# Optimization experiments

Measured on AMD Instinct MI355X. Metric: run time of the kernel, lower is better.

The kernel has to match this reference:

```python
import jax, jax.numpy as jnp
import numpy as np

TOP_K = 2  # num_experts_per_token


def setup_inputs() -> dict:
    key = jax.random.key(0)
    ks = jax.random.split(key, 6)
    B, S, H, F, E = 4, 2048, 1024, 4096, 8  # F = 2 * intermediate_size
    scale = 0.02
    x = jax.random.normal(ks[0], (B, S, H), dtype=jnp.float32)
    gate_w = jax.random.normal(ks[1], (E, H), dtype=jnp.float32) * scale
    w1 = jax.random.normal(ks[2], (E, H, F), dtype=jnp.float32) * scale
    b1 = jnp.zeros((E, F), dtype=jnp.float32)
    w2 = jax.random.normal(ks[3], (E, F, H), dtype=jnp.float32) * scale
    b2 = jnp.zeros((E, H), dtype=jnp.float32)
    return {"x": x, "gate_w": gate_w, "w1": w1, "b1": b1, "w2": w2, "b2": b2}


def reference(x, gate_w, w1, b1, w2, b2):
    # x: [B, S, H]; gate_w: [E, H]; w1: [E, H, F]; b1: [E, F]; w2: [E, F, H]; b2: [E, H]
    E = gate_w.shape[0]
    gate_logits = jnp.einsum('bsh,eh->bse', x, gate_w)
    gate_probs = jax.nn.softmax(gate_logits, axis=-1)
    top_v, top_i = jax.lax.top_k(gate_probs, TOP_K)  # [B, S, K]
    # Combine weight per expert: w[b,s,e] = sum_k top_v[b,s,k] * (top_i[b,s,k] == e)
    onehot = jax.nn.one_hot(top_i, E, dtype=x.dtype)          # [B, S, K, E]
    comb_w = jnp.einsum('bsk,bske->bse', top_v, onehot)       # [B, S, E]
    out = jnp.zeros_like(x)
    for e in range(E):  # small fixed expert loop
        h = jax.nn.silu(jnp.einsum('bsh,hf->bsf', x, w1[e]) + b1[e])
        y = jnp.einsum('bsf,fh->bsh', h, w2[e]) + b2[e]
        out = out + y * comb_w[..., e:e + 1]
    return out
```

## Files before the change

### kernel.cpp

```cpp
#include <hip/hip_runtime.h>
#include <stdint.h>

#define T_TOK 8192
#define HDIM  1024
#define FDIM  4096
#define NEXP  8
#define BT    256
#define RCAP  (2*T_TOK + NEXP*256)
#define LDSB  65536

typedef short  short8  __attribute__((ext_vector_type(8)));
typedef unsigned short ushort8 __attribute__((ext_vector_type(8)));
typedef float  f32x4   __attribute__((ext_vector_type(4)));

#define MFMA __builtin_amdgcn_mfma_f32_16x16x32_bf16

__device__ __forceinline__ unsigned short f2bf(float f) {
  unsigned u = __float_as_uint(f);
  u += 0x7fffu + ((u >> 16) & 1u);
  return (unsigned short)(u >> 16);
}
__device__ __forceinline__ float bf2f(unsigned short u) {
  return __uint_as_float((unsigned)u << 16);
}

__device__ __forceinline__ void gload16(const void* g, void* l) {
  __builtin_amdgcn_global_load_lds(
      (const __attribute__((address_space(1))) void*)g,
      (__attribute__((address_space(3))) void*)l, 16, 0, 0);
}

__global__ __launch_bounds__(256) void k_transp_cvt(const float* __restrict__ in,
                                                    unsigned short* __restrict__ out,
                                                    int K, int N) {
  __shared__ unsigned short s[64][72];
  const float* ine = in + (size_t)blockIdx.z * K * N;
  unsigned short* oute = out + (size_t)blockIdx.z * K * N;
  int k0 = blockIdx.y * 64, n0 = blockIdx.x * 64;
  int t = threadIdx.x;
  int kr = t >> 4, nc = (t & 15) * 4;
#pragma unroll
  for (int it = 0; it < 4; ++it) {
    int k = it * 16 + kr;
    float4 v = *(const float4*)(ine + (size_t)(k0 + k) * N + n0 + nc);
    ushort4 u = make_ushort4(f2bf(v.x), f2bf(v.y), f2bf(v.z), f2bf(v.w));
    *(ushort4*)(&s[k][nc]) = u;
  }
  __syncthreads();
  int nr = t >> 3, kc = (t & 7) * 8;
#pragma unroll
  for (int v = 0; v < 2; ++v) {
    int n = v * 32 + nr;
    ushort8 o;
#pragma unroll
    for (int j = 0; j < 8; ++j) o[j] = s[kc + j][n];
    *(ushort8*)(oute + (size_t)(n0 + n) * K + k0 + kc) = o;
  }
}

__global__ void k_gate(const float* __restrict__ x, const float* __restrict__ gw,
                       unsigned short* __restrict__ xb,
                       int2* __restrict__ eidx, float2* __restrict__ ewt) {
  int tid = threadIdx.x;
  int lane = tid & 63;
  int t = blockIdx.x * 4 + (tid >> 6);
  const float* xr = x + (size_t)t * HDIM;
  unsigned short* xbr = xb + (size_t)t * HDIM;
  float acc[NEXP];
#pragma unroll
  for (int e = 0; e < NEXP; e++) acc[e] = 0.f;
#pragma unroll
  for (int i = 0; i < HDIM / 64; i++) {
    float xv = xr[i * 64 + lane];
    xbr[i * 64 + lane] = f2bf(xv);
#pragma unroll
    for (int e = 0; e < NEXP; e++) acc[e] += xv * gw[e * HDIM + i * 64 + lane];
  }
#pragma unroll
  for (int e = 0; e < NEXP; e++) {
    acc[e] += __shfl_xor(acc[e], 32);
    acc[e] += __shfl_xor(acc[e], 16);
    acc[e] += __shfl_xor(acc[e], 8);
    acc[e] += __shfl_xor(acc[e], 4);
    acc[e] += __shfl_xor(acc[e], 2);
    acc[e] += __shfl_xor(acc[e], 1);
  }
  float m = acc[0];
#pragma unroll
  for (int e = 1; e < NEXP; e++) m = fmaxf(m, acc[e]);
  float p[NEXP]; float s = 0.f;
#pragma unroll
  for (int e = 0; e < NEXP; e++) { p[e] = expf(acc[e] - m); s += p[e]; }
  float inv = 1.f / s;
#pragma unroll
  for (int e = 0; e < NEXP; e++) p[e] *= inv;
  int b0 = 0; float v0 = p[0];
#pragma unroll
  for (int e = 1; e < NEXP; e++) if (p[e] > v0) { v0 = p[e]; b0 = e; }
  int b1i = (b0 == 0) ? 1 : 0; float v1 = p[b1i];
#pragma unroll
  for (int e = 0; e < NEXP; e++) if (e != b0 && p[e] > v1) { v1 = p[e]; b1i = e; }
  if (lane == 0) { eidx[t] = make_int2(b0, b1i); ewt[t] = make_float2(v0, v1); }
}

__global__ void k_compact(const int2* __restrict__ eidx,
                          int* __restrict__ list_tok, int* __restrict__ counts) {
  int e = blockIdx.x;
  int tid = threadIdx.x, lane = tid & 63, wid = tid >> 6;
  __shared__ int sbase;
  __shared__ int wcnt[4];
  if (tid == 0) sbase = 0;
  __syncthreads();
  for (int c = 0; c < T_TOK; c += 256) {
    int t = c + tid;
    int2 ei = eidx[t];
    bool sel = (ei.x == e) || (ei.y == e);
    unsigned long long b = __ballot(sel);
    if (lane == 0) wcnt[wid] = __popcll(b);
    __syncthreads();
    int pre = sbase;
    for (int w = 0; w < wid; w++) pre += wcnt[w];
    int pos = pre + __popcll(b & ((1ull << lane) - 1ull));
    if (sel) list_tok[e * T_TOK + pos] = t;
    __syncthreads();
    if (tid == 0) sbase += wcnt[0] + wcnt[1] + wcnt[2] + wcnt[3];
    __syncthreads();
  }
  if (tid == 0) counts[e] = sbase;
}

__global__ void k_offsets(const int* __restrict__ counts, int* __restrict__ off_pad) {
  if (threadIdx.x == 0) {
    int o = 0;
    off_pad[0] = 0;
    for (int e = 0; e < NEXP; e++) {
      o += ((counts[e] + BT - 1) / BT) * BT;
      off_pad[e + 1] = o;
    }
  }
}

__global__ void k_invert(const int* __restrict__ list_tok, const int* __restrict__ counts,
                         const int* __restrict__ off_pad, const int2* __restrict__ eidx,
                         int2* __restrict__ tok2slot) {
  int e = blockIdx.y;
  int p = blockIdx.x * 256 + threadIdx.x;
  if (p < counts[e]) {
    int t = list_tok[e * T_TOK + p];
    int slot = off_pad[e] + p;
    if (eidx[t].x == e) tok2slot[t].x = slot;
    else                tok2slot[t].y = slot;
  }
}

#define STAGE_A(u_, v_) { \
    char* lb_ = smem + (((v_)&1) ? LDSB : 0) + (u_)*16384; \
    gload16(gA[u_][0] + (size_t)(v_)*128, lb_ + dst0); \
    gload16(gA[u_][1] + (size_t)(v_)*128, lb_ + dst1); }
#define STAGE_B(u_, v_) { \
    char* lb_ = smem + (((v_)&1) ? LDSB : 0) + 32768 + (u_)*16384; \
    gload16(gB[u_][0] + (size_t)(v_)*128, lb_ + dst0); \
    gload16(gB[u_][1] + (size_t)(v_)*128, lb_ + dst1); }

#define PHASE2(M0_, M1_, M2_, M3_, STAGE_STMT, TAIL_STMT) { \
    short8 a0l = *(const short8*)(pA0 + (M0_)*2048), a0h = *(const short8*)(pA1 + (M0_)*2048); \
    short8 a1l = *(const short8*)(pA0 + (M1_)*2048), a1h = *(const short8*)(pA1 + (M1_)*2048); \
    short8 a2l = *(const short8*)(pA0 + (M2_)*2048), a2h = *(const short8*)(pA1 + (M2_)*2048); \
    short8 a3l = *(const short8*)(pA0 + (M3_)*2048), a3h = *(const short8*)(pA1 + (M3_)*2048); \
    STAGE_STMT; \
    __builtin_amdgcn_s_barrier(); \
    asm volatile("s_waitcnt lgkmcnt(0)" ::: "memory"); \
    __builtin_amdgcn_sched_barrier(0); \
    __builtin_amdgcn_s_setprio(1); \
    acc[M0_][0] = MFMA(a0l, b00, acc[M0_][0], 0,0,0); \
    acc[M0_][1] = MFMA(a0l, b10, acc[M0_][1], 0,0,0); \
    acc[M0_][2] = MFMA(a0l, b20, acc[M0_][2], 0,0,0); \
    acc[M0_][3] = MFMA(a0l, b30, acc[M0_][3], 0,0,0); \
    acc[M1_][0] = MFMA(a1l, b00, acc[M1_][0], 0,0,0); \
    acc[M1_][1] = MFMA(a1l, b10, acc[M1_][1], 0,0,0); \
    acc[M1_][2] = MFMA(a1l, b20, acc[M1_][2], 0,0,0); \
    acc[M1_][3] = MFMA(a1l, b30, acc[M1_][3], 0,0,0); \
    acc[M2_][0] = MFMA(a2l, b00, acc[M2_][0], 0,0,0); \
    acc[M2_][1] = MFMA(a2l, b10, acc[M2_][1], 0,0,0); \
    acc[M2_][2] = MFMA(a2l, b20, acc[M2_][2], 0,0,0); \
    acc[M2_][3] = MFMA(a2l, b30, acc[M2_][3], 0,0,0); \
    acc[M3_][0] = MFMA(a3l, b00, acc[M3_][0], 0,0,0); \
    acc[M3_][1] = MFMA(a3l, b10, acc[M3_][1], 0,0,0); \
    acc[M3_][2] = MFMA(a3l, b20, acc[M3_][2], 0,0,0); \
    acc[M3_][3] = MFMA(a3l, b30, acc[M3_][3], 0,0,0); \
    acc[M0_][0] = MFMA(a0h, b01, acc[M0_][0], 0,0,0); \
    acc[M0_][1] = MFMA(a0h, b11, acc[M0_][1], 0,0,0); \
    acc[M0_][2] = MFMA(a0h, b21, acc[M0_][2], 0,0,0); \
    acc[M0_][3] = MFMA(a0h, b31, acc[M0_][3], 0,0,0); \
    acc[M1_][0] = MFMA(a1h, b01, acc[M1_][0], 0,0,0); \
    acc[M1_][1] = MFMA(a1h, b11, acc[M1_][1], 0,0,0); \
    acc[M1_][2] = MFMA(a1h, b21, acc[M1_][2], 0,0,0); \
    acc[M1_][3] = MFMA(a1h, b31, acc[M1_][3], 0,0,0); \
    acc[M2_][0] = MFMA(a2h, b01, acc[M2_][0], 0,0,0); \
    acc[M2_][1] = MFMA(a2h, b11, acc[M2_][1], 0,0,0); \
    acc[M2_][2] = MFMA(a2h, b21, acc[M2_][2], 0,0,0); \
    acc[M2_][3] = MFMA(a2h, b31, acc[M2_][3], 0,0,0); \
    acc[M3_][0] = MFMA(a3h, b01, acc[M3_][0], 0,0,0); \
    acc[M3_][1] = MFMA(a3h, b11, acc[M3_][1], 0,0,0); \
    acc[M3_][2] = MFMA(a3h, b21, acc[M3_][2], 0,0,0); \
    acc[M3_][3] = MFMA(a3h, b31, acc[M3_][3], 0,0,0); \
    __builtin_amdgcn_s_setprio(0); \
    TAIL_STMT; \
    __builtin_amdgcn_s_barrier(); }

#define READ_B4 \
    short8 b00 = *(const short8*)(pB0),        b01 = *(const short8*)(pB1); \
    short8 b10 = *(const short8*)(pB0 + 2048), b11 = *(const short8*)(pB1 + 2048); \
    short8 b20 = *(const short8*)(pB0 + 4096), b21 = *(const short8*)(pB1 + 4096); \
    short8 b30 = *(const short8*)(pB0 + 6144), b31 = *(const short8*)(pB1 + 6144);

#define GEMM_TILE_LOOP(NT) \
  STAGE_A(0,0); STAGE_A(1,0); STAGE_B(0,0); STAGE_B(1,0); STAGE_B(0,1); STAGE_B(1,1); \
  asm volatile("s_waitcnt vmcnt(4)" ::: "memory"); \
  __builtin_amdgcn_s_barrier(); \
  for (int v = 0; v < (NT); ++v) { \
    const char* bufb = smem + ((v&1) ? LDSB : 0); \
    const char* pA0 = bufb + wm * 16384 + aoff0; \
    const char* pA1 = bufb + wm * 16384 + aoff1; \
    const char* pB0 = bufb + 32768 + (wn >> 1) * 16384 + boff0; \
    const char* pB1 = bufb + 32768 + (wn >> 1) * 16384 + boff1; \
    READ_B4; \
    PHASE2(0, 1, 2, 3, { if (v+1 < (NT)) { STAGE_A(0, v+1); STAGE_A(1, v+1); } }, {}); \
    PHASE2(4, 5, 6, 7, { if (v+2 < (NT)) { STAGE_B(0, v+2); STAGE_B(1, v+2); } }, { \
      if (v+2 < (NT))      { asm volatile("s_waitcnt vmcnt(4)" ::: "memory"); } \
      else if (v+1 < (NT)) { asm volatile("s_waitcnt vmcnt(0)" ::: "memory"); } }); \
  }

__global__ __launch_bounds__(512, 2) void k_gemm1(
    const unsigned short* __restrict__ xb, const unsigned short* __restrict__ w1t,
    const float* __restrict__ b1, const int* __restrict__ list_tok,
    const int* __restrict__ counts, const int* __restrict__ off_pad,
    unsigned short* __restrict__ h) {
  extern __shared__ char smem[];
  int wl = (blockIdx.x & 7) * 144 + (blockIdx.x >> 3);
  int r0 = (wl >> 4) * BT;
  int n0 = (wl & 15) * BT;
  if (r0 >= off_pad[NEXP]) return;
  int e = 0;
#pragma unroll
  for (int i = 0; i < NEXP; ++i) if (r0 >= off_pad[i + 1]) e = i + 1;
  int base = off_pad[e], cnt = counts[e];

  int t = threadIdx.x, l = t & 63, w = t >> 6;
  int wm = w >> 2, wn = w & 3;
  int lr = l & 15, g16 = (l >> 4) * 16;
  int swz = (lr & 7) << 4;
  int aoff0 = lr * 128 + (g16 ^ swz);
  int aoff1 = lr * 128 + ((64 + g16) ^ swz);
  int boff0 = (wn & 1) * 8192 + aoff0;
  int boff1 = (wn & 1) * 8192 + aoff1;

  int dst0 = t * 16, dst1 = t * 16 + 8192;
  int srow = t >> 3;
  int skb = (((t & 7) ^ ((t >> 3) & 7)) << 4);
  const char* gA[2][2];
  const char* gB[2][2];
#pragma unroll
  for (int u = 0; u < 2; ++u)
#pragma unroll
    for (int j = 0; j < 2; ++j) {
      int row = u * 128 + srow + 64 * j;
      int se = r0 - base + row;
      int tok = (se < cnt) ? list_tok[e * T_TOK + se] : 0;
      gA[u][j] = (const char*)(xb + (size_t)tok * HDIM) + skb;
      gB[u][j] = (const char*)(w1t + (size_t)e * FDIM * HDIM + (size_t)(n0 + row) * HDIM) + skb;
    }

  f32x4 acc[8][4];
#pragma unroll
  for (int m = 0; m < 8; ++m)
#pragma unroll
    for (int n = 0; n < 4; ++n) acc[m][n] = (f32x4){0.f, 0.f, 0.f, 0.f};

  GEMM_TILE_LOOP(HDIM / 64);

  const float* b1e = b1 + (size_t)e * FDIM + n0;
  unsigned short* Cs = (unsigned short*)smem;
  int lh = l >> 4, lh4 = lh * 4;
  int cswz = lh << 4;
#pragma unroll
  for (int n = 0; n < 4; ++n) {
    int col = wn * 64 + n * 16 + lr;
    int colX = col ^ cswz;
    float bv = b1e[col];
#pragma unroll
    for (int m = 0; m < 8; ++m) {
      int row = wm * 128 + m * 16 + lh4;
#pragma unroll
      for (int i = 0; i < 4; ++i) {
        float vv = acc[m][n][i] + bv;
        float sg = __builtin_amdgcn_rcpf(1.f + __expf(-vv));
        Cs[(size_t)(row + i) * BT + colX] = f2bf(vv * sg);
      }
    }
  }
  __syncthreads();
#pragma unroll
  for (int s = 0; s < 16; ++s) {
    int lin = s * 512 + t;
    int row = lin >> 5, c8 = (lin & 31) * 8;
    int c8X = c8 ^ (((row >> 2) & 3) << 4);
    *(ushort8*)(h + (size_t)(r0 + row) * FDIM + n0 + c8) = *(const ushort8*)(Cs + (size_t)row * BT + c8X);
  }
}

__global__ __launch_bounds__(512, 2) void k_gemm2(
    const unsigned short* __restrict__ h, const unsigned short* __restrict__ w2t,
    const float* __restrict__ b2, const int* __restrict__ off_pad,
    unsigned short* __restrict__ ypartA, unsigned short* __restrict__ ypartB) {
  extern __shared__ char smem[];
  int wl = (blockIdx.x & 7) * 72 + (blockIdx.x >> 3);
  int mB = wl >> 3, rem = wl & 7;
  int r0 = mB * BT;
  int n0 = (rem >> 1) * BT;
  int z  = rem & 1;
  if (r0 >= off_pad[NEXP]) return;
  int e = 0;
#pragma unroll
  for (int i = 0; i < NEXP; ++i) if (r0 >= off_pad[i + 1]) e = i + 1;

  int t = threadIdx.x, l = t & 63, w = t >> 6;
  int wm = w >> 2, wn = w & 3;
  int lr = l & 15, g16 = (l >> 4) * 16;
  int swz = (lr & 7) << 4;
  int aoff0 = lr * 128 + (g16 ^ swz);
  int aoff1 = lr * 128 + ((64 + g16) ^ swz);
  int boff0 = (wn & 1) * 8192 + aoff0;
  int boff1 = (wn & 1) * 8192 + aoff1;

  int dst0 = t * 16, dst1 = t * 16 + 8192;
  int srow = t >> 3;
  int skb = (((t & 7) ^ ((t >> 3) & 7)) << 4);
  const char* gA[2][2];
  const char* gB[2][2];
#pragma unroll
  for (int u = 0; u < 2; ++u)
#pragma unroll
    for (int j = 0; j < 2; ++j) {
      int row = u * 128 + srow + 64 * j;
      gA[u][j] = (const char*)(h + (size_t)(r0 + row) * FDIM + (size_t)z * 2048) + skb;
      gB[u][j] = (const char*)(w2t + (size_t)e * HDIM * FDIM + (size_t)(n0 + row) * FDIM + (size_t)z * 2048) + skb;
    }

  f32x4 acc[8][4];
#pragma unroll
  for (int m = 0; m < 8; ++m)
#pragma unroll
    for (int n = 0; n < 4; ++n) acc[m][n] = (f32x4){0.f, 0.f, 0.f, 0.f};

  GEMM_TILE_LOOP(2048 / 64);

  const float* b2e = b2 + (size_t)e * HDIM + n0;
  unsigned short* yp = z ? ypartB : ypartA;
  unsigned short* Cs = (unsigned short*)smem;
  int lh = l >> 4, lh4 = lh * 4;
  int cswz = lh << 4;
#pragma unroll
  for (int n = 0; n < 4; ++n) {
    int col = wn * 64 + n * 16 + lr;
    int colX = col ^ cswz;
    float bv = (z == 0) ? b2e[col] : 0.f;
#pragma unroll
    for (int m = 0; m < 8; ++m) {
      int row = wm * 128 + m * 16 + lh4;
#pragma unroll
      for (int i = 0; i < 4; ++i)
        Cs[(size_t)(row + i) * BT + colX] = f2bf(acc[m][n][i] + bv);
    }
  }
  __syncthreads();
#pragma unroll
  for (int s = 0; s < 16; ++s) {
    int lin = s * 512 + t;
    int row = lin >> 5, c8 = (lin & 31) * 8;
    int c8X = c8 ^ (((row >> 2) & 3) << 4);
    *(ushort8*)(yp + (size_t)(r0 + row) * HDIM + n0 + c8) = *(const ushort8*)(Cs + (size_t)row * BT + c8X);
  }
}

__global__ void k_reduce(const unsigned short* __restrict__ ypartA,
                         const unsigned short* __restrict__ ypartB,
                         const int2* __restrict__ tok2slot, const float2* __restrict__ ewt,
                         float* __restrict__ out) {
  int idx = blockIdx.x * 256 + threadIdx.x;
  int t = idx >> 7;
  int c8 = (idx & 127) * 8;
  int2 s = tok2slot[t];
  float2 wv = ewt[t];
  ushort8 a0 = *(const ushort8*)(ypartA + (size_t)s.x * HDIM + c8);
  ushort8 a1 = *(const ushort8*)(ypartB + (size_t)s.x * HDIM + c8);
  ushort8 b0 = *(const ushort8*)(ypartA + (size_t)s.y * HDIM + c8);
  ushort8 b1 = *(const ushort8*)(ypartB + (size_t)s.y * HDIM + c8);
  float o[8];
#pragma unroll
  for (int j = 0; j < 8; ++j)
    o[j] = wv.x * (bf2f((unsigned short)a0[j]) + bf2f((unsigned short)a1[j]))
         + wv.y * (bf2f((unsigned short)b0[j]) + bf2f((unsigned short)b1[j]));
  float* op = out + (size_t)t * HDIM + c8;
  *(float4*)op = make_float4(o[0], o[1], o[2], o[3]);
  *(float4*)(op + 4) = make_float4(o[4], o[5], o[6], o[7]);
}

extern "C" void kernel_launch(void* const* d_in, const int* in_sizes, int n_in,
                              void* d_out, int out_size, void* d_ws, size_t ws_size,
                              hipStream_t stream) {
  const float* x  = (const float*)d_in[0];
  const float* gw = (const float*)d_in[1];
  const float* w1 = (const float*)d_in[2];
  const float* b1 = (const float*)d_in[3];
  const float* w2 = (const float*)d_in[4];
  const float* b2 = (const float*)d_in[5];
  float* out = (float*)d_out;

  char* ws = (char*)d_ws;
  size_t off = 0;
  unsigned short* xb = (unsigned short*)(ws + off); off += (size_t)T_TOK * HDIM * 2;
  int2*   eidx = (int2*)(ws + off);   off += (size_t)T_TOK * 8;
  float2* ewt  = (float2*)(ws + off); off += (size_t)T_TOK * 8;
  int2* tok2slot = (int2*)(ws + off); off += (size_t)T_TOK * 8;
  int*  list_tok = (int*)(ws + off);  off += (size_t)NEXP * T_TOK * 4;
  int* counts  = (int*)(ws + off); off += 64;
  int* off_pad = (int*)(ws + off); off += 64;
  off = (off + 255) & ~(size_t)255;
  unsigned short* h      = (unsigned short*)(ws + off); off += (size_t)RCAP * FDIM * 2;
  unsigned short* wT     = (unsigned short*)(ws + off); off += (size_t)NEXP * HDIM * FDIM * 2;
  unsigned short* ypartA = (unsigned short*)(ws + off); off += (size_t)RCAP * HDIM * 2;
  unsigned short* ypartB = (unsigned short*)(ws + off); off += (size_t)RCAP * HDIM * 2;
  if (ws_size < off) return;

  hipFuncSetAttribute((const void*)k_gemm1, hipFuncAttributeMaxDynamicSharedMemorySize, 131072);
  hipFuncSetAttribute((const void*)k_gemm2, hipFuncAttributeMaxDynamicSharedMemorySize, 131072);

  k_gate<<<T_TOK / 4, 256, 0, stream>>>(x, gw, xb, eidx, ewt);
  k_compact<<<NEXP, 256, 0, stream>>>(eidx, list_tok, counts);
  k_offsets<<<1, 64, 0, stream>>>(counts, off_pad);
  k_invert<<<dim3(T_TOK / 256, NEXP), 256, 0, stream>>>(list_tok, counts, off_pad, eidx, tok2slot);
  k_transp_cvt<<<dim3(FDIM / 64, HDIM / 64, NEXP), 256, 0, stream>>>(w1, wT, HDIM, FDIM);
  k_gemm1<<<8 * 144, 512, 131072, stream>>>(xb, wT, b1, list_tok, counts, off_pad, h);
  k_transp_cvt<<<dim3(HDIM / 64, FDIM / 64, NEXP), 256, 0, stream>>>(w2, wT, FDIM, HDIM);
  k_gemm2<<<8 * 72, 512, 131072, stream>>>(h, wT, b2, off_pad, ypartA, ypartB);
  k_reduce<<<T_TOK * (HDIM / 8) / 256, 256, 0, stream>>>(ypartA, ypartB, tok2slot, ewt, out);
}
```

Before: 512.5 us.

## Vectorize gate loads, widen compaction blocks, drop explicit waitcnt/setprio in GEMM loop

The gate kernel now reads x and gate weights as float4 and writes the bf16 copy as ushort4, cutting the number of memory instructions. The compaction kernel uses 1024-thread blocks, so it needs a quarter as many barrier-separated iterations. In the GEMM main loop the explicit lgkmcnt(0) wait, sched_barrier and setprio are replaced by compiler memory fences. That hands LDS-read wait placement to the compiler, which could help or hurt the MFMA overlap.

```diff
diff --git a/kernel.cpp b/kernel.cpp
--- a/kernel.cpp
+++ b/kernel.cpp
@@ -70,11 +70,15 @@
 #pragma unroll
   for (int e = 0; e < NEXP; e++) acc[e] = 0.f;
 #pragma unroll
-  for (int i = 0; i < HDIM / 64; i++) {
-    float xv = xr[i * 64 + lane];
-    xbr[i * 64 + lane] = f2bf(xv);
-#pragma unroll
-    for (int e = 0; e < NEXP; e++) acc[e] += xv * gw[e * HDIM + i * 64 + lane];
+  for (int i = 0; i < 4; i++) {
+    int idx = i * 256 + lane * 4;
+    float4 xv = *(const float4*)(xr + idx);
+    *(ushort4*)(xbr + idx) = make_ushort4(f2bf(xv.x), f2bf(xv.y), f2bf(xv.z), f2bf(xv.w));
+#pragma unroll
+    for (int e = 0; e < NEXP; e++) {
+      float4 gv = *(const float4*)(gw + e * HDIM + idx);
+      acc[e] += xv.x * gv.x + xv.y * gv.y + xv.z * gv.z + xv.w * gv.w;
+    }
   }
 #pragma unroll
   for (int e = 0; e < NEXP; e++) {
@@ -103,15 +107,15 @@
   if (lane == 0) { eidx[t] = make_int2(b0, b1i); ewt[t] = make_float2(v0, v1); }
 }
 
-__global__ void k_compact(const int2* __restrict__ eidx,
+__global__ __launch_bounds__(1024) void k_compact(const int2* __restrict__ eidx,
                           int* __restrict__ list_tok, int* __restrict__ counts) {
   int e = blockIdx.x;
   int tid = threadIdx.x, lane = tid & 63, wid = tid >> 6;
   __shared__ int sbase;
-  __shared__ int wcnt[4];
+  __shared__ int wcnt[16];
   if (tid == 0) sbase = 0;
   __syncthreads();
-  for (int c = 0; c < T_TOK; c += 256) {
+  for (int c = 0; c < T_TOK; c += 1024) {
     int t = c + tid;
     int2 ei = eidx[t];
     bool sel = (ei.x == e) || (ei.y == e);
@@ -123,7 +127,11 @@
     int pos = pre + __popcll(b & ((1ull << lane) - 1ull));
     if (sel) list_tok[e * T_TOK + pos] = t;
     __syncthreads();
-    if (tid == 0) sbase += wcnt[0] + wcnt[1] + wcnt[2] + wcnt[3];
+    if (tid == 0) {
+      int tot = 0;
+      for (int w = 0; w < 16; w++) tot += wcnt[w];
+      sbase += tot;
+    }
     __syncthreads();
   }
   if (tid == 0) counts[e] = sbase;
@@ -153,6 +161,8 @@
   }
 }
 
+#define CFENCE asm volatile("" ::: "memory")
+
 #define STAGE_A(u_, v_) { \
     char* lb_ = smem + (((v_)&1) ? LDSB : 0) + (u_)*16384; \
     gload16(gA[u_][0] + (size_t)(v_)*128, lb_ + dst0); \
@@ -168,10 +178,9 @@
     short8 a2l = *(const short8*)(pA0 + (M2_)*2048), a2h = *(const short8*)(pA1 + (M2_)*2048); \
     short8 a3l = *(const short8*)(pA0 + (M3_)*2048), a3h = *(const short8*)(pA1 + (M3_)*2048); \
     STAGE_STMT; \
+    CFENCE; \
     __builtin_amdgcn_s_barrier(); \
-    asm volatile("s_waitcnt lgkmcnt(0)" ::: "memory"); \
-    __builtin_amdgcn_sched_barrier(0); \
-    __builtin_amdgcn_s_setprio(1); \
+    CFENCE; \
     acc[M0_][0] = MFMA(a0l, b00, acc[M0_][0], 0,0,0); \
     acc[M0_][1] = MFMA(a0l, b10, acc[M0_][1], 0,0,0); \
     acc[M0_][2] = MFMA(a0l, b20, acc[M0_][2], 0,0,0); \
@@ -204,9 +213,10 @@
     acc[M3_][1] = MFMA(a3h, b11, acc[M3_][1], 0,0,0); \
     acc[M3_][2] = MFMA(a3h, b21, acc[M3_][2], 0,0,0); \
     acc[M3_][3] = MFMA(a3h, b31, acc[M3_][3], 0,0,0); \
-    __builtin_amdgcn_s_setprio(0); \
     TAIL_STMT; \
-    __builtin_amdgcn_s_barrier(); }
+    CFENCE; \
+    __builtin_amdgcn_s_barrier(); \
+    CFENCE; }
 
 #define READ_B4 \
     short8 b00 = *(const short8*)(pB0),        b01 = *(const short8*)(pB1); \
@@ -218,6 +228,7 @@
   STAGE_A(0,0); STAGE_A(1,0); STAGE_B(0,0); STAGE_B(1,0); STAGE_B(0,1); STAGE_B(1,1); \
   asm volatile("s_waitcnt vmcnt(4)" ::: "memory"); \
   __builtin_amdgcn_s_barrier(); \
+  CFENCE; \
   for (int v = 0; v < (NT); ++v) { \
     const char* bufb = smem + ((v&1) ? LDSB : 0); \
     const char* pA0 = bufb + wm * 16384 + aoff0; \
@@ -437,7 +448,7 @@
   hipFuncSetAttribute((const void*)k_gemm2, hipFuncAttributeMaxDynamicSharedMemorySize, 131072);
 
   k_gate<<<T_TOK / 4, 256, 0, stream>>>(x, gw, xb, eidx, ewt);
-  k_compact<<<NEXP, 256, 0, stream>>>(eidx, list_tok, counts);
+  k_compact<<<NEXP, 1024, 0, stream>>>(eidx, list_tok, counts);
   k_offsets<<<1, 64, 0, stream>>>(counts, off_pad);
   k_invert<<<dim3(T_TOK / 256, NEXP), 256, 0, stream>>>(list_tok, counts, off_pad, eidx, tok2slot);
   k_transp_cvt<<<dim3(FDIM / 64, HDIM / 64, NEXP), 256, 0, stream>>>(w1, wT, HDIM, FDIM);
```

New measurement: 464.3 us. 9.4% less time.
